# Optimization experiments

Hardware: AMD Instinct MI355X
Metric: run time of the kernel (lower is better)

Reference implementation:

```python
import jax, jax.numpy as jnp
import numpy as np

N_ACTIVE = 100000
C = 64
N_BLOCKS = 2
K = 27  # 3x3x3 submanifold rulebook offsets
BN_EPS = 1e-4  # scn BatchNorm default eps


def setup_inputs() -> dict:
    key = jax.random.key(0)
    k1, k2, k3 = jax.random.split(key, 3)
    feats = jax.random.normal(k1, (N_ACTIVE, C), dtype=jnp.float32)
    # rulebook: index N_ACTIVE == missing neighbor (points at padded zero row)
    nbrs = jax.random.randint(k2, (N_ACTIVE, K), 0, N_ACTIVE + 1, dtype=jnp.int32)
    # make the center offset (k=13) point at self, as in a real submanifold rulebook
    nbrs = nbrs.at[:, K // 2].set(jnp.arange(N_ACTIVE, dtype=jnp.int32))
    fan_in = K * C
    W = jax.random.normal(k3, (N_BLOCKS, 2, K, C, C), dtype=jnp.float32) / np.sqrt(fan_in)
    gamma = jnp.ones((N_BLOCKS, 2, C), dtype=jnp.float32)
    beta = jnp.zeros((N_BLOCKS, 2, C), dtype=jnp.float32)
    return {"feats": feats, "nbrs": nbrs, "W": W, "gamma": gamma, "beta": beta}


def _subm_conv(x, nbrs, Wk):
    # x: [N, C]; nbrs: [N, K] with value N meaning 'missing'; Wk: [K, C, C]
    x_pad = jnp.concatenate([x, jnp.zeros((1, x.shape[1]), x.dtype)], axis=0)
    g = x_pad[nbrs]  # [N, K, C] rulebook gather
    return jnp.einsum('nkc,kcd->nd', g, Wk)  # gather-GEMM-scatter fused by contraction


def _bn(x, g, b):
    mu = jnp.mean(x, axis=0)
    var = jnp.var(x, axis=0)
    return (x - mu) * jax.lax.rsqrt(var + BN_EPS) * g + b


def reference(feats, nbrs, W, gamma, beta):
    x = feats
    for i in range(N_BLOCKS):  # SparseResidualBlock chain
        residual = x
        out = _subm_conv(x, nbrs, W[i, 0])
        out = jax.nn.relu(_bn(out, gamma[i, 0], beta[i, 0]))  # BatchNormReLU
        out = _subm_conv(out, nbrs, W[i, 1])
        out = _bn(out, gamma[i, 1], beta[i, 1])  # BatchNormalization
        x = jax.nn.relu(out + residual)  # AddTable + ReLU
    return x
```

## Files before the change

### kernel.cpp

```cpp
#include <hip/hip_runtime.h>

#define N_PTS 100000
#define NT_STRIDE 100096
#define NK 27
#define NKP 28
#define TOTAL (N_PTS * 64)
#define NB_CONV 1564

typedef short bf16x8 __attribute__((ext_vector_type(8)));
typedef float f32x4 __attribute__((ext_vector_type(4)));
typedef unsigned short u16x8 __attribute__((ext_vector_type(8)));

__device__ __forceinline__ unsigned short f2bf(float f) {
    unsigned u = __builtin_bit_cast(unsigned, f);
    u += 0x7fffu + ((u >> 16) & 1u);
    return (unsigned short)(u >> 16);
}
__device__ __forceinline__ float bf2f(unsigned short u) {
    return __builtin_bit_cast(float, ((unsigned)u) << 16);
}

__global__ void cast_in_k(const float* __restrict__ feats, unsigned short* __restrict__ xb) {
    int t = blockIdx.x * 256 + threadIdx.x;
    if (t >= (N_PTS + 1) * 8) return;
    int i = t * 8;
    u16x8 o;
    if (i < TOTAL) {
        f32x4 v0 = ((const f32x4*)(feats + i))[0];
        f32x4 v1 = ((const f32x4*)(feats + i))[1];
#pragma unroll
        for (int j = 0; j < 4; ++j) { o[j] = f2bf(v0[j]); o[4 + j] = f2bf(v1[j]); }
    } else {
#pragma unroll
        for (int j = 0; j < 8; ++j) o[j] = 0;
    }
    *(u16x8*)(xb + i) = o;
}

__global__ void tr_nbrs_k(const int* __restrict__ nbrs, int* __restrict__ nbrsT) {
    __shared__ int tile[64 * 28];
    const int n0 = blockIdx.x * 64;
    const int t = threadIdx.x;
    const int base = n0 * 27;
    for (int i = t; i < 1728; i += 256) {
        int v = (base + i < N_PTS * 27) ? nbrs[base + i] : N_PTS;
        int r = i / 27, c = i - r * 27;
        tile[r * 28 + c] = v;
    }
    __syncthreads();
    for (int i = t; i < 1728; i += 256) {
        int k = i >> 6, j = i & 63;
        nbrsT[(size_t)k * NT_STRIDE + n0 + j] = tile[j * 28 + k];
    }
    for (int i = t; i < 64; i += 256)
        nbrsT[(size_t)27 * NT_STRIDE + n0 + i] = N_PTS;
}

__global__ void pack_w_k(const float* __restrict__ W, unsigned short* __restrict__ Wp) {
    int o = blockIdx.x * 256 + threadIdx.x;
    if (o >= 4 * NKP * 4096) return;
    int conv = o / (NKP * 4096);
    int r = o - conv * (NKP * 4096);
    int k = r >> 12;
    if (k == 27) { Wp[o] = 0; return; }
    int r2 = r & 4095;
    int frag = r2 >> 9;
    int kk = frag >> 2, cb = frag & 3;
    int lane = (r2 >> 3) & 63;
    int j = r2 & 7;
    int c = kk * 32 + (lane >> 4) * 8 + j;
    int d = cb * 16 + (lane & 15);
    Wp[o] = f2bf(W[(size_t)(conv * NK + k) * 4096 + c * 64 + d]);
}

#define SLAB_HW 72
#define SLAB_SZ (32 * SLAB_HW)
__global__ __launch_bounds__(256, 4) void conv_k(
    const unsigned short* __restrict__ xin,
    const int* __restrict__ nbrsT,
    const unsigned short* __restrict__ Wp,
    unsigned short* __restrict__ yout,
    float* __restrict__ gpart_out)
{
    const int tid = threadIdx.x;
    const int lane = tid & 63;
    const int wave = tid >> 6;
    const int l15 = lane & 15;
    const int lgrp = lane >> 4;
    const int oct = lane >> 3;
    const int chk = lane & 7;
    const int h = wave & 1;
    const int kh = wave >> 1;
    const int wave_row = blockIdx.x * 64 + h * 32;
    const int k0 = kh * 14;

    __shared__ __align__(16) float smem[9216];
    __shared__ __align__(16) float sred[4][128];
    unsigned short* slab = (unsigned short*)smem + wave * (2 * SLAB_SZ);
    float* ytile = smem;

    f32x4 acc[2][4];
#pragma unroll
    for (int m = 0; m < 2; ++m)
#pragma unroll
        for (int cb = 0; cb < 4; ++cb) acc[m][cb] = (f32x4)0.f;

    const bf16x8* wp = (const bf16x8*)Wp;

    int idxP[4], idxN[4];
    bf16x8 gv[2][4];

#pragma unroll
    for (int i = 0; i < 4; ++i)
        idxP[i] = nbrsT[(size_t)k0 * NT_STRIDE + wave_row + i * 8 + oct];
#pragma unroll
    for (int i = 0; i < 4; ++i)
        idxN[i] = nbrsT[(size_t)(k0 + 1) * NT_STRIDE + wave_row + i * 8 + oct];
#pragma unroll
    for (int i = 0; i < 4; ++i)
        gv[0][i] = *(const bf16x8*)(xin + (size_t)idxP[i] * 64 + chk * 8);
#pragma unroll
    for (int i = 0; i < 4; ++i)
        *(bf16x8*)(slab + (i * 8 + oct) * SLAB_HW + chk * 8) = gv[0][i];
#pragma unroll
    for (int i = 0; i < 4; ++i)
        gv[1][i] = *(const bf16x8*)(xin + (size_t)idxN[i] * 64 + chk * 8);

#pragma unroll
    for (int s = 0; s < 14; ++s) {
        if (s + 2 < 14) {
#pragma unroll
            for (int i = 0; i < 4; ++i)
                idxP[i] = nbrsT[(size_t)(k0 + s + 2) * NT_STRIDE + wave_row + i * 8 + oct];
        }
        if (s + 1 < 14) {
#pragma unroll
            for (int i = 0; i < 4; ++i)
                *(bf16x8*)(slab + ((s + 1) & 1) * SLAB_SZ + (i * 8 + oct) * SLAB_HW + chk * 8) = gv[(s + 1) & 1][i];
        }
        if (s + 2 < 14) {
#pragma unroll
            for (int i = 0; i < 4; ++i)
                gv[s & 1][i] = *(const bf16x8*)(xin + (size_t)idxP[i] * 64 + chk * 8);
        }
        const unsigned short* sb = slab + (s & 1) * SLAB_SZ;
        bf16x8 a00 = *(const bf16x8*)(sb + l15 * SLAB_HW + lgrp * 8);
        bf16x8 a01 = *(const bf16x8*)(sb + l15 * SLAB_HW + 32 + lgrp * 8);
        bf16x8 a10 = *(const bf16x8*)(sb + (16 + l15) * SLAB_HW + lgrp * 8);
        bf16x8 a11 = *(const bf16x8*)(sb + (16 + l15) * SLAB_HW + 32 + lgrp * 8);

        const bf16x8* wk = wp + (size_t)(k0 + s) * 512 + lane;
        {
            bf16x8 b0 = wk[0], b1 = wk[64], b2 = wk[128], b3 = wk[192];
            acc[0][0] = __builtin_amdgcn_mfma_f32_16x16x32_bf16(a00, b0, acc[0][0], 0, 0, 0);
            acc[1][0] = __builtin_amdgcn_mfma_f32_16x16x32_bf16(a10, b0, acc[1][0], 0, 0, 0);
            acc[0][1] = __builtin_amdgcn_mfma_f32_16x16x32_bf16(a00, b1, acc[0][1], 0, 0, 0);
            acc[1][1] = __builtin_amdgcn_mfma_f32_16x16x32_bf16(a10, b1, acc[1][1], 0, 0, 0);
            acc[0][2] = __builtin_amdgcn_mfma_f32_16x16x32_bf16(a00, b2, acc[0][2], 0, 0, 0);
            acc[1][2] = __builtin_amdgcn_mfma_f32_16x16x32_bf16(a10, b2, acc[1][2], 0, 0, 0);
            acc[0][3] = __builtin_amdgcn_mfma_f32_16x16x32_bf16(a00, b3, acc[0][3], 0, 0, 0);
            acc[1][3] = __builtin_amdgcn_mfma_f32_16x16x32_bf16(a10, b3, acc[1][3], 0, 0, 0);
        }
        {
            bf16x8 b0 = wk[256], b1 = wk[320], b2 = wk[384], b3 = wk[448];
            acc[0][0] = __builtin_amdgcn_mfma_f32_16x16x32_bf16(a01, b0, acc[0][0], 0, 0, 0);
            acc[1][0] = __builtin_amdgcn_mfma_f32_16x16x32_bf16(a11, b0, acc[1][0], 0, 0, 0);
            acc[0][1] = __builtin_amdgcn_mfma_f32_16x16x32_bf16(a01, b1, acc[0][1], 0, 0, 0);
            acc[1][1] = __builtin_amdgcn_mfma_f32_16x16x32_bf16(a11, b1, acc[1][1], 0, 0, 0);
            acc[0][2] = __builtin_amdgcn_mfma_f32_16x16x32_bf16(a01, b2, acc[0][2], 0, 0, 0);
            acc[1][2] = __builtin_amdgcn_mfma_f32_16x16x32_bf16(a11, b2, acc[1][2], 0, 0, 0);
            acc[0][3] = __builtin_amdgcn_mfma_f32_16x16x32_bf16(a01, b3, acc[0][3], 0, 0, 0);
            acc[1][3] = __builtin_amdgcn_mfma_f32_16x16x32_bf16(a11, b3, acc[1][3], 0, 0, 0);
        }
    }

    __syncthreads();

    if (kh == 0) {
#pragma unroll
        for (int m = 0; m < 2; ++m)
#pragma unroll
            for (int cb = 0; cb < 4; ++cb)
#pragma unroll
                for (int r = 0; r < 4; ++r)
                    ytile[(h * 32 + m * 16 + lgrp * 4 + r) * 68 + cb * 16 + l15] = acc[m][cb][r];
    }
    __syncthreads();
    if (kh == 1) {
#pragma unroll
        for (int m = 0; m < 2; ++m)
#pragma unroll
            for (int cb = 0; cb < 4; ++cb)
#pragma unroll
                for (int r = 0; r < 4; ++r)
                    ytile[(h * 32 + m * 16 + lgrp * 4 + r) * 68 + cb * 16 + l15] += acc[m][cb][r];
    }
    __syncthreads();

    const int row = tid >> 2;
    const int colb = (tid & 3) * 16;
    f32x4 v[4];
#pragma unroll
    for (int j = 0; j < 4; ++j) v[j] = *(const f32x4*)&ytile[row * 68 + colb + 4 * j];

    const int grow = blockIdx.x * 64 + row;
    if (grow < N_PTS) {
        u16x8 o0, o1;
#pragma unroll
        for (int j = 0; j < 4; ++j) { o0[j] = f2bf(v[0][j]); o0[4 + j] = f2bf(v[1][j]); }
#pragma unroll
        for (int j = 0; j < 4; ++j) { o1[j] = f2bf(v[2][j]); o1[4 + j] = f2bf(v[3][j]); }
        *(u16x8*)(yout + (size_t)grow * 64 + colb) = o0;
        *(u16x8*)(yout + (size_t)grow * 64 + colb + 8) = o1;
    }

    f32x4 sv[4], s2v[4];
#pragma unroll
    for (int j = 0; j < 4; ++j) { sv[j] = v[j]; s2v[j] = v[j] * v[j]; }
#pragma unroll
    for (int off = 4; off < 64; off <<= 1) {
#pragma unroll
        for (int j = 0; j < 4; ++j) {
#pragma unroll
            for (int e = 0; e < 4; ++e) {
                sv[j][e]  += __shfl_xor(sv[j][e],  off);
                s2v[j][e] += __shfl_xor(s2v[j][e], off);
            }
        }
    }
    if (lane < 4) {
#pragma unroll
        for (int j = 0; j < 4; ++j) {
            *(f32x4*)&sred[wave][lane * 16 + 4 * j]      = sv[j];
            *(f32x4*)&sred[wave][64 + lane * 16 + 4 * j] = s2v[j];
        }
    }
    __syncthreads();
    if (tid < 128) {
        float p = sred[0][tid] + sred[1][tid] + sred[2][tid] + sred[3][tid];
        atomicAdd(&gpart_out[tid], p);
    }
}

__global__ void bn_relu_cast_k(const unsigned short* __restrict__ yraw,
                               const float* __restrict__ gpart,
                               const float* __restrict__ gamma,
                               const float* __restrict__ beta,
                               unsigned short* __restrict__ xb) {
    int t = blockIdx.x * 256 + threadIdx.x;
    if (t >= TOTAL / 8) return;
    int i = t * 8;
    int c0 = i & 63;
    u16x8 v = *(const u16x8*)(yraw + i);
    const float invN = 1.0f / (float)N_PTS;
    u16x8 o;
#pragma unroll
    for (int j = 0; j < 8; ++j) {
        int c = c0 + j;
        float S = gpart[c], S2 = gpart[64 + c];
        float mu = S * invN;
        float var = S2 * invN - mu * mu;
        float s = gamma[c] * rsqrtf(var + 1e-4f);
        o[j] = f2bf(fmaxf(bf2f(v[j]) * s + (beta[c] - mu * s), 0.f));
    }
    *(u16x8*)(xb + i) = o;
}

__global__ void bn_add_relu_k(const unsigned short* __restrict__ yraw,
                              const float* __restrict__ gpart,
                              const float* __restrict__ gamma,
                              const float* __restrict__ beta,
                              const float* __restrict__ res,
                              float* __restrict__ xout,
                              unsigned short* __restrict__ xb, int writeBf) {
    int t = blockIdx.x * 256 + threadIdx.x;
    if (t >= TOTAL / 8) return;
    int i = t * 8;
    int c0 = i & 63;
    u16x8 v = *(const u16x8*)(yraw + i);
    f32x4 q0 = ((const f32x4*)(res + i))[0];
    f32x4 q1 = ((const f32x4*)(res + i))[1];
    const float invN = 1.0f / (float)N_PTS;
    float ov[8];
#pragma unroll
    for (int j = 0; j < 8; ++j) {
        int c = c0 + j;
        float S = gpart[c], S2 = gpart[64 + c];
        float mu = S * invN;
        float var = S2 * invN - mu * mu;
        float s = gamma[c] * rsqrtf(var + 1e-4f);
        float q = (j < 4) ? q0[j] : q1[j - 4];
        ov[j] = fmaxf(bf2f(v[j]) * s + (beta[c] - mu * s) + q, 0.f);
    }
    f32x4 o0, o1;
#pragma unroll
    for (int j = 0; j < 4; ++j) { o0[j] = ov[j]; o1[j] = ov[4 + j]; }
    ((f32x4*)(xout + i))[0] = o0;
    ((f32x4*)(xout + i))[1] = o1;
    if (writeBf) {
        u16x8 o;
#pragma unroll
        for (int j = 0; j < 8; ++j) o[j] = f2bf(ov[j]);
        *(u16x8*)(xb + i) = o;
    }
}

extern "C" void kernel_launch(void* const* d_in, const int* in_sizes, int n_in,
                              void* d_out, int out_size, void* d_ws, size_t ws_size,
                              hipStream_t stream) {
    const float* feats = (const float*)d_in[0];
    const int*   nbrs  = (const int*)d_in[1];
    const float* W     = (const float*)d_in[2];
    const float* gamma = (const float*)d_in[3];
    const float* beta  = (const float*)d_in[4];
    float* out = (float*)d_out;

    char* ws = (char*)d_ws;
    unsigned short* xb    = (unsigned short*)ws;
    unsigned short* ybf   = (unsigned short*)(ws + 12800512);
    unsigned short* Wp    = (unsigned short*)(ws + 25600512);
    int*            nbrsT = (int*)(ws + 26518016);
    float*          gpart = (float*)(ws + 37728768);

    dim3 b256(256);
    hipMemsetAsync(gpart, 0, 4 * 128 * sizeof(float), stream);
    cast_in_k<<<((N_PTS + 1) * 8 + 255) / 256, b256, 0, stream>>>(feats, xb);
    tr_nbrs_k<<<NT_STRIDE / 64, b256, 0, stream>>>(nbrs, nbrsT);
    pack_w_k<<<(4 * NKP * 4096) / 256, b256, 0, stream>>>(W, Wp);

    const int appl_blocks = (TOTAL / 8) / 256;
    for (int blk = 0; blk < 2; ++blk) {
        const int c0 = blk * 2, c1 = blk * 2 + 1;
        conv_k<<<NB_CONV, b256, 0, stream>>>(
            xb, nbrsT, Wp + (size_t)c0 * NKP * 4096, ybf, gpart + c0 * 128);
        bn_relu_cast_k<<<appl_blocks, b256, 0, stream>>>(
            ybf, gpart + c0 * 128, gamma + c0 * 64, beta + c0 * 64, xb);
        conv_k<<<NB_CONV, b256, 0, stream>>>(
            xb, nbrsT, Wp + (size_t)c1 * NKP * 4096, ybf, gpart + c1 * 128);
        const float* resp = (blk == 0) ? feats : (const float*)out;
        bn_add_relu_k<<<appl_blocks, b256, 0, stream>>>(
            ybf, gpart + c1 * 128, gamma + c1 * 64, beta + c1 * 64, resp, out, xb, blk == 0 ? 1 : 0);
    }
}
```

Before: 444.8 us.

## Store activations as per-row int8 and dequantize in registers inside conv gather

Activations between convolutions are quantized to int8 with a per-row fp32 scale instead of being stored as bf16. The conv kernel now gathers int8 rows straight from global memory into registers, with a deeper index and data prefetch, and dequantizes them to bf16 on the fly. This removes the LDS staging slab and halves the gather bytes. The final residual add also reads the int8 copy, which saves fp32 traffic but adds quantization error to the output and extra ALU work for dequantization.

```diff
diff --git a/kernel.cpp b/kernel.cpp
--- a/kernel.cpp
+++ b/kernel.cpp
@@ -10,6 +10,7 @@
 typedef short bf16x8 __attribute__((ext_vector_type(8)));
 typedef float f32x4 __attribute__((ext_vector_type(4)));
 typedef unsigned short u16x8 __attribute__((ext_vector_type(8)));
+typedef char i8x8 __attribute__((ext_vector_type(8)));
 
 __device__ __forceinline__ unsigned short f2bf(float f) {
     unsigned u = __builtin_bit_cast(unsigned, f);
@@ -19,22 +20,45 @@
 __device__ __forceinline__ float bf2f(unsigned short u) {
     return __builtin_bit_cast(float, ((unsigned)u) << 16);
 }
-
-__global__ void cast_in_k(const float* __restrict__ feats, unsigned short* __restrict__ xb) {
+__device__ __forceinline__ bf16x8 dq8(i8x8 q, float s) {
+    u16x8 o;
+#pragma unroll
+    for (int j = 0; j < 8; ++j) {
+        float f = (float)q[j] * s;
+        unsigned u = __builtin_bit_cast(unsigned, f) + 0x8000u;
+        o[j] = (unsigned short)(u >> 16);
+    }
+    return __builtin_bit_cast(bf16x8, o);
+}
+
+__global__ void cast_in_k(const float* __restrict__ feats, char* __restrict__ xq,
+                          float* __restrict__ stbl) {
     int t = blockIdx.x * 256 + threadIdx.x;
     if (t >= (N_PTS + 1) * 8) return;
     int i = t * 8;
-    u16x8 o;
-    if (i < TOTAL) {
-        f32x4 v0 = ((const f32x4*)(feats + i))[0];
-        f32x4 v1 = ((const f32x4*)(feats + i))[1];
-#pragma unroll
-        for (int j = 0; j < 4; ++j) { o[j] = f2bf(v0[j]); o[4 + j] = f2bf(v1[j]); }
-    } else {
-#pragma unroll
-        for (int j = 0; j < 8; ++j) o[j] = 0;
-    }
-    *(u16x8*)(xb + i) = o;
+    int row = t >> 3;
+    if (row >= N_PTS) {
+        *(i8x8*)(xq + i) = (i8x8)(char)0;
+        if ((t & 7) == 0) stbl[row] = 0.f;
+        return;
+    }
+    f32x4 v0 = ((const f32x4*)(feats + i))[0];
+    f32x4 v1 = ((const f32x4*)(feats + i))[1];
+    float m = 0.f;
+#pragma unroll
+    for (int j = 0; j < 4; ++j) m = fmaxf(m, fmaxf(fabsf(v0[j]), fabsf(v1[j])));
+    m = fmaxf(m, __shfl_xor(m, 1));
+    m = fmaxf(m, __shfl_xor(m, 2));
+    m = fmaxf(m, __shfl_xor(m, 4));
+    float inv = (m > 0.f) ? 127.0f / m : 0.f;
+    i8x8 q;
+#pragma unroll
+    for (int j = 0; j < 4; ++j) {
+        q[j]     = (char)(int)rintf(v0[j] * inv);
+        q[4 + j] = (char)(int)rintf(v1[j] * inv);
+    }
+    *(i8x8*)(xq + i) = q;
+    if ((t & 7) == 0) stbl[row] = m * (1.0f / 127.0f);
 }
 
 __global__ void tr_nbrs_k(const int* __restrict__ nbrs, int* __restrict__ nbrsT) {
@@ -73,13 +97,12 @@
     Wp[o] = f2bf(W[(size_t)(conv * NK + k) * 4096 + c * 64 + d]);
 }
 
-#define SLAB_HW 72
-#define SLAB_SZ (32 * SLAB_HW)
 __global__ __launch_bounds__(256, 4) void conv_k(
-    const unsigned short* __restrict__ xin,
+    const char* __restrict__ xq,
+    const float* __restrict__ stbl,
     const int* __restrict__ nbrsT,
     const unsigned short* __restrict__ Wp,
-    unsigned short* __restrict__ yout,
+    unsigned short* __restrict__ ybf,
     float* __restrict__ gpart_out)
 {
     const int tid = threadIdx.x;
@@ -87,18 +110,13 @@
     const int wave = tid >> 6;
     const int l15 = lane & 15;
     const int lgrp = lane >> 4;
-    const int oct = lane >> 3;
-    const int chk = lane & 7;
     const int h = wave & 1;
     const int kh = wave >> 1;
     const int wave_row = blockIdx.x * 64 + h * 32;
+    const int r0 = wave_row + l15;
+    const int r1 = r0 + 16;
     const int k0 = kh * 14;
 
-    __shared__ __align__(16) float smem[9216];
-    __shared__ __align__(16) float sred[4][128];
-    unsigned short* slab = (unsigned short*)smem + wave * (2 * SLAB_SZ);
-    float* ytile = smem;
-
     f32x4 acc[2][4];
 #pragma unroll
     for (int m = 0; m < 2; ++m)
@@ -107,48 +125,44 @@
 
     const bf16x8* wp = (const bf16x8*)Wp;
 
-    int idxP[4], idxN[4];
-    bf16x8 gv[2][4];
-
-#pragma unroll
-    for (int i = 0; i < 4; ++i)
-        idxP[i] = nbrsT[(size_t)k0 * NT_STRIDE + wave_row + i * 8 + oct];
-#pragma unroll
-    for (int i = 0; i < 4; ++i)
-        idxN[i] = nbrsT[(size_t)(k0 + 1) * NT_STRIDE + wave_row + i * 8 + oct];
-#pragma unroll
-    for (int i = 0; i < 4; ++i)
-        gv[0][i] = *(const bf16x8*)(xin + (size_t)idxP[i] * 64 + chk * 8);
-#pragma unroll
-    for (int i = 0; i < 4; ++i)
-        *(bf16x8*)(slab + (i * 8 + oct) * SLAB_HW + chk * 8) = gv[0][i];
-#pragma unroll
-    for (int i = 0; i < 4; ++i)
-        gv[1][i] = *(const bf16x8*)(xin + (size_t)idxN[i] * 64 + chk * 8);
+    int id0[4], id1[4];
+#pragma unroll
+    for (int s = 0; s < 4; ++s) {
+        id0[s] = nbrsT[(size_t)(k0 + s) * NT_STRIDE + r0];
+        id1[s] = nbrsT[(size_t)(k0 + s) * NT_STRIDE + r1];
+    }
+    i8x8 qpf[3][4];
+    float spf[3][2];
+#pragma unroll
+    for (int s = 0; s < 2; ++s) {
+        const i8x8* p0 = (const i8x8*)(xq + (size_t)id0[s] * 64);
+        const i8x8* p1 = (const i8x8*)(xq + (size_t)id1[s] * 64);
+        qpf[s][0] = p0[lgrp]; qpf[s][1] = p0[4 + lgrp];
+        qpf[s][2] = p1[lgrp]; qpf[s][3] = p1[4 + lgrp];
+        spf[s][0] = stbl[id0[s]]; spf[s][1] = stbl[id1[s]];
+    }
 
 #pragma unroll
     for (int s = 0; s < 14; ++s) {
+        if (s + 4 < 14) {
+            id0[s & 3] = nbrsT[(size_t)(k0 + s + 4) * NT_STRIDE + r0];
+            id1[s & 3] = nbrsT[(size_t)(k0 + s + 4) * NT_STRIDE + r1];
+        }
         if (s + 2 < 14) {
-#pragma unroll
-            for (int i = 0; i < 4; ++i)
-                idxP[i] = nbrsT[(size_t)(k0 + s + 2) * NT_STRIDE + wave_row + i * 8 + oct];
-        }
-        if (s + 1 < 14) {
-#pragma unroll
-            for (int i = 0; i < 4; ++i)
-                *(bf16x8*)(slab + ((s + 1) & 1) * SLAB_SZ + (i * 8 + oct) * SLAB_HW + chk * 8) = gv[(s + 1) & 1][i];
-        }
-        if (s + 2 < 14) {
-#pragma unroll
-            for (int i = 0; i < 4; ++i)
-                gv[s & 1][i] = *(const bf16x8*)(xin + (size_t)idxP[i] * 64 + chk * 8);
-        }
-        const unsigned short* sb = slab + (s & 1) * SLAB_SZ;
-        bf16x8 a00 = *(const bf16x8*)(sb + l15 * SLAB_HW + lgrp * 8);
-        bf16x8 a01 = *(const bf16x8*)(sb + l15 * SLAB_HW + 32 + lgrp * 8);
-        bf16x8 a10 = *(const bf16x8*)(sb + (16 + l15) * SLAB_HW + lgrp * 8);
-        bf16x8 a11 = *(const bf16x8*)(sb + (16 + l15) * SLAB_HW + 32 + lgrp * 8);
-
+            const int j = (s + 2) & 3;
+            const int st2 = (s + 2) % 3;
+            const i8x8* p0 = (const i8x8*)(xq + (size_t)id0[j] * 64);
+            const i8x8* p1 = (const i8x8*)(xq + (size_t)id1[j] * 64);
+            qpf[st2][0] = p0[lgrp]; qpf[st2][1] = p0[4 + lgrp];
+            qpf[st2][2] = p1[lgrp]; qpf[st2][3] = p1[4 + lgrp];
+            spf[st2][0] = stbl[id0[j]]; spf[st2][1] = stbl[id1[j]];
+        }
+        __builtin_amdgcn_sched_barrier(0);
+        const int st = s % 3;
+        bf16x8 a00 = dq8(qpf[st][0], spf[st][0]);
+        bf16x8 a01 = dq8(qpf[st][1], spf[st][0]);
+        bf16x8 a10 = dq8(qpf[st][2], spf[st][1]);
+        bf16x8 a11 = dq8(qpf[st][3], spf[st][1]);
         const bf16x8* wk = wp + (size_t)(k0 + s) * 512 + lane;
         {
             bf16x8 b0 = wk[0], b1 = wk[64], b2 = wk[128], b3 = wk[192];
@@ -174,7 +188,8 @@
         }
     }
 
-    __syncthreads();
+    __shared__ __align__(16) float ytile[64 * 68];
+    __shared__ __align__(16) float sred[4][128];
 
     if (kh == 0) {
 #pragma unroll
@@ -210,8 +225,8 @@
         for (int j = 0; j < 4; ++j) { o0[j] = f2bf(v[0][j]); o0[4 + j] = f2bf(v[1][j]); }
 #pragma unroll
         for (int j = 0; j < 4; ++j) { o1[j] = f2bf(v[2][j]); o1[4 + j] = f2bf(v[3][j]); }
-        *(u16x8*)(yout + (size_t)grow * 64 + colb) = o0;
-        *(u16x8*)(yout + (size_t)grow * 64 + colb + 8) = o1;
+        *(u16x8*)(ybf + (size_t)grow * 64 + colb) = o0;
+        *(u16x8*)(ybf + (size_t)grow * 64 + colb + 8) = o1;
     }
 
     f32x4 sv[4], s2v[4];
@@ -242,18 +257,25 @@
     }
 }
 
-__global__ void bn_relu_cast_k(const unsigned short* __restrict__ yraw,
-                               const float* __restrict__ gpart,
-                               const float* __restrict__ gamma,
-                               const float* __restrict__ beta,
-                               unsigned short* __restrict__ xb) {
+__global__ void bn_relu_quant_k(const unsigned short* __restrict__ yraw,
+                                const float* __restrict__ gpart,
+                                const float* __restrict__ gamma,
+                                const float* __restrict__ beta,
+                                char* __restrict__ xq, float* __restrict__ stbl) {
     int t = blockIdx.x * 256 + threadIdx.x;
-    if (t >= TOTAL / 8) return;
+    if (t >= (N_PTS + 1) * 8) return;
     int i = t * 8;
+    int row = t >> 3;
+    if (row >= N_PTS) {
+        *(i8x8*)(xq + i) = (i8x8)(char)0;
+        if ((t & 7) == 0) stbl[row] = 0.f;
+        return;
+    }
     int c0 = i & 63;
     u16x8 v = *(const u16x8*)(yraw + i);
     const float invN = 1.0f / (float)N_PTS;
-    u16x8 o;
+    float ov[8];
+    float m = 0.f;
 #pragma unroll
     for (int j = 0; j < 8; ++j) {
         int c = c0 + j;
@@ -261,27 +283,37 @@
         float mu = S * invN;
         float var = S2 * invN - mu * mu;
         float s = gamma[c] * rsqrtf(var + 1e-4f);
-        o[j] = f2bf(fmaxf(bf2f(v[j]) * s + (beta[c] - mu * s), 0.f));
-    }
-    *(u16x8*)(xb + i) = o;
-}
-
-__global__ void bn_add_relu_k(const unsigned short* __restrict__ yraw,
-                              const float* __restrict__ gpart,
-                              const float* __restrict__ gamma,
-                              const float* __restrict__ beta,
-                              const float* __restrict__ res,
-                              float* __restrict__ xout,
-                              unsigned short* __restrict__ xb, int writeBf) {
+        ov[j] = fmaxf(bf2f(v[j]) * s + (beta[c] - mu * s), 0.f);
+        m = fmaxf(m, ov[j]);
+    }
+    m = fmaxf(m, __shfl_xor(m, 1));
+    m = fmaxf(m, __shfl_xor(m, 2));
+    m = fmaxf(m, __shfl_xor(m, 4));
+    float inv = (m > 0.f) ? 127.0f / m : 0.f;
+    i8x8 q;
+#pragma unroll
+    for (int j = 0; j < 8; ++j) q[j] = (char)(int)rintf(ov[j] * inv);
+    *(i8x8*)(xq + i) = q;
+    if ((t & 7) == 0) stbl[row] = m * (1.0f / 127.0f);
+}
+
+__global__ void bn_add_relu_quant_k(const unsigned short* __restrict__ yraw,
+                                    const float* __restrict__ gpart,
+                                    const float* __restrict__ gamma,
+                                    const float* __restrict__ beta,
+                                    const float* __restrict__ res,
+                                    char* __restrict__ xq, float* __restrict__ stbl) {
     int t = blockIdx.x * 256 + threadIdx.x;
     if (t >= TOTAL / 8) return;
     int i = t * 8;
+    int row = t >> 3;
     int c0 = i & 63;
     u16x8 v = *(const u16x8*)(yraw + i);
     f32x4 q0 = ((const f32x4*)(res + i))[0];
     f32x4 q1 = ((const f32x4*)(res + i))[1];
     const float invN = 1.0f / (float)N_PTS;
     float ov[8];
+    float m = 0.f;
 #pragma unroll
     for (int j = 0; j < 8; ++j) {
         int c = c0 + j;
@@ -289,20 +321,51 @@
         float mu = S * invN;
         float var = S2 * invN - mu * mu;
         float s = gamma[c] * rsqrtf(var + 1e-4f);
-        float q = (j < 4) ? q0[j] : q1[j - 4];
-        ov[j] = fmaxf(bf2f(v[j]) * s + (beta[c] - mu * s) + q, 0.f);
-    }
+        float r = (j < 4) ? q0[j] : q1[j - 4];
+        ov[j] = fmaxf(bf2f(v[j]) * s + (beta[c] - mu * s) + r, 0.f);
+        m = fmaxf(m, ov[j]);
+    }
+    m = fmaxf(m, __shfl_xor(m, 1));
+    m = fmaxf(m, __shfl_xor(m, 2));
+    m = fmaxf(m, __shfl_xor(m, 4));
+    float inv = (m > 0.f) ? 127.0f / m : 0.f;
+    i8x8 q;
+#pragma unroll
+    for (int j = 0; j < 8; ++j) q[j] = (char)(int)rintf(ov[j] * inv);
+    *(i8x8*)(xq + i) = q;
+    if ((t & 7) == 0) stbl[row] = m * (1.0f / 127.0f);
+}
+
+__global__ void bn_add_relu_final_k(const unsigned short* __restrict__ yraw,
+                                    const float* __restrict__ gpart,
+                                    const float* __restrict__ gamma,
+                                    const float* __restrict__ beta,
+                                    const char* __restrict__ resq,
+                                    const float* __restrict__ res_stbl,
+                                    float* __restrict__ xout) {
+    int t = blockIdx.x * 256 + threadIdx.x;
+    if (t >= TOTAL / 8) return;
+    int i = t * 8;
+    int row = t >> 3;
+    int c0 = i & 63;
+    u16x8 v = *(const u16x8*)(yraw + i);
+    i8x8 rq = *(const i8x8*)(resq + i);
+    float rs = res_stbl[row];
+    const float invN = 1.0f / (float)N_PTS;
     f32x4 o0, o1;
 #pragma unroll
-    for (int j = 0; j < 4; ++j) { o0[j] = ov[j]; o1[j] = ov[4 + j]; }
+    for (int j = 0; j < 8; ++j) {
+        int c = c0 + j;
+        float S = gpart[c], S2 = gpart[64 + c];
+        float mu = S * invN;
+        float var = S2 * invN - mu * mu;
+        float s = gamma[c] * rsqrtf(var + 1e-4f);
+        float r = (float)rq[j] * rs;
+        float o = fmaxf(bf2f(v[j]) * s + (beta[c] - mu * s) + r, 0.f);
+        if (j < 4) o0[j] = o; else o1[j - 4] = o;
+    }
     ((f32x4*)(xout + i))[0] = o0;
     ((f32x4*)(xout + i))[1] = o1;
-    if (writeBf) {
-        u16x8 o;
-#pragma unroll
-        for (int j = 0; j < 8; ++j) o[j] = f2bf(ov[j]);
-        *(u16x8*)(xb + i) = o;
-    }
 }
 
 extern "C" void kernel_launch(void* const* d_in, const int* in_sizes, int n_in,
@@ -316,29 +379,37 @@
     float* out = (float*)d_out;
 
     char* ws = (char*)d_ws;
-    unsigned short* xb    = (unsigned short*)ws;
-    unsigned short* ybf   = (unsigned short*)(ws + 12800512);
-    unsigned short* Wp    = (unsigned short*)(ws + 25600512);
-    int*            nbrsT = (int*)(ws + 26518016);
-    float*          gpart = (float*)(ws + 37728768);
+    char*           xq0   = ws;
+    float*          stbl0 = (float*)(ws + 6400128);
+    char*           xq1   = ws + 6800144;
+    float*          stbl1 = (float*)(ws + 13200272);
+    unsigned short* ybf   = (unsigned short*)(ws + 13600288);
+    unsigned short* Wp    = (unsigned short*)(ws + 26400288);
+    int*            nbrsT = (int*)(ws + 27317792);
+    float*          gpart = (float*)(ws + 38528544);
 
     dim3 b256(256);
     hipMemsetAsync(gpart, 0, 4 * 128 * sizeof(float), stream);
-    cast_in_k<<<((N_PTS + 1) * 8 + 255) / 256, b256, 0, stream>>>(feats, xb);
+    const int qrows_blocks = ((N_PTS + 1) * 8 + 255) / 256;
+    cast_in_k<<<qrows_blocks, b256, 0, stream>>>(feats, xq0, stbl0);
     tr_nbrs_k<<<NT_STRIDE / 64, b256, 0, stream>>>(nbrs, nbrsT);
     pack_w_k<<<(4 * NKP * 4096) / 256, b256, 0, stream>>>(W, Wp);
 
-    const int appl_blocks = (TOTAL / 8) / 256;
+    const int appl_blocks = (TOTAL / 8 + 255) / 256;
     for (int blk = 0; blk < 2; ++blk) {
         const int c0 = blk * 2, c1 = blk * 2 + 1;
         conv_k<<<NB_CONV, b256, 0, stream>>>(
-            xb, nbrsT, Wp + (size_t)c0 * NKP * 4096, ybf, gpart + c0 * 128);
-        bn_relu_cast_k<<<appl_blocks, b256, 0, stream>>>(
-            ybf, gpart + c0 * 128, gamma + c0 * 64, beta + c0 * 64, xb);
+            xq0, stbl0, nbrsT, Wp + (size_t)c0 * NKP * 4096, ybf, gpart + c0 * 128);
+        bn_relu_quant_k<<<qrows_blocks, b256, 0, stream>>>(
+            ybf, gpart + c0 * 128, gamma + c0 * 64, beta + c0 * 64, xq1, stbl1);
         conv_k<<<NB_CONV, b256, 0, stream>>>(
-            xb, nbrsT, Wp + (size_t)c1 * NKP * 4096, ybf, gpart + c1 * 128);
-        const float* resp = (blk == 0) ? feats : (const float*)out;
-        bn_add_relu_k<<<appl_blocks, b256, 0, stream>>>(
-            ybf, gpart + c1 * 128, gamma + c1 * 64, beta + c1 * 64, resp, out, xb, blk == 0 ? 1 : 0);
-    }
-}
+            xq1, stbl1, nbrsT, Wp + (size_t)c1 * NKP * 4096, ybf, gpart + c1 * 128);
+        if (blk == 0) {
+            bn_add_relu_quant_k<<<appl_blocks, b256, 0, stream>>>(
+                ybf, gpart + c1 * 128, gamma + c1 * 64, beta + c1 * 64, feats, xq0, stbl0);
+        } else {
+            bn_add_relu_final_k<<<appl_blocks, b256, 0, stream>>>(
+                ybf, gpart + c1 * 128, gamma + c1 * 64, beta + c1 * 64, xq0, stbl0, out);
+        }
+    }
+}
```

New measurement: 868.5 us. 95.3% more time.
